# Kernel optimization log

Measured on AMD Instinct MI355X. Metric: run time of the kernel, lower is better.

The kernel has to match this reference:

```python
import jax, jax.numpy as jnp
import numpy as np

N = 50000      # nodes
F_IN = 128     # num_feat
HID = 128      # hidden size
OUT = 47       # num_out (classes)
E = 600000     # graph edges
EGO_E = 1200000  # concatenated egonet edges


def _linear_params(key, fan_in, fan_out):
    s = 1.0 / np.sqrt(fan_in)
    kw, kb = jax.random.split(key)
    W = jax.random.uniform(kw, (fan_in, fan_out), jnp.float32, -s, s)
    b = jax.random.uniform(kb, (fan_out,), jnp.float32, -s, s)
    return W, b


def setup_inputs() -> dict:
    key = jax.random.key(0)
    ks = jax.random.split(key, 8)
    x_in = jax.random.normal(ks[0], (N, F_IN), jnp.float32)
    edge_index_in = jax.random.randint(ks[1], (2, E), 0, N)
    ego_edge_index = jax.random.randint(ks[2], (2, EGO_E), 0, N)
    W_ego0, b_ego0 = _linear_params(ks[3], F_IN, F_IN)
    W_gin0, b_gin0 = _linear_params(ks[4], F_IN, HID)
    W_ego1, b_ego1 = _linear_params(ks[5], HID, HID)
    W_gin1, b_gin1 = _linear_params(ks[6], HID, OUT)
    return {
        "x_in": x_in, "edge_index_in": edge_index_in, "ego_edge_index": ego_edge_index,
        "W_ego0": W_ego0, "b_ego0": b_ego0, "W_gin0": W_gin0, "b_gin0": b_gin0,
        "W_ego1": W_ego1, "b_ego1": b_ego1, "W_gin1": W_gin1, "b_gin1": b_gin1,
    }


def reference(x_in, edge_index_in, ego_edge_index,
              W_ego0, b_ego0, W_gin0, b_gin0,
              W_ego1, b_ego1, W_gin1, b_gin1):
    n = x_in.shape[0]
    ego_row, ego_col = ego_edge_index[0], ego_edge_index[1]
    src, tgt = edge_index_in[0], edge_index_in[1]

    def do_conv(x):
        # sum_i spmm(A_i, x) == scatter-add over concatenated egonet edges, then / N
        return jax.ops.segment_sum(x[ego_col], ego_row, num_segments=n) * (1.0 / n)

    def gin(x, W, b):
        # GINConv(nn=Linear), eps=0: Linear(x + sum_{j->i} x_j)
        aggr = jax.ops.segment_sum(x[src], tgt, num_segments=n)
        return (x + aggr) @ W + b

    # layer 0: ['Ego','GIN', relu_mid=True, relu_end=True]
    x = do_conv(x_in) @ W_ego0 + b_ego0
    x = jax.nn.relu(x)
    x = gin(x, W_gin0, b_gin0)
    x = jax.nn.relu(x)
    # layer 1: ['Ego','GIN', relu_mid=True, relu_end=False]
    x = do_conv(x) @ W_ego1 + b_ego1
    x = jax.nn.relu(x)
    x = gin(x, W_gin1, b_gin1)
    return jax.nn.log_softmax(x, axis=1)
```

## Files before the change

kernel.cpp:

```cpp
#include <hip/hip_runtime.h>

#define SCAP_EGO 8192
#define SCAP_E   4096

typedef unsigned short ushort_t;
typedef unsigned int uint_t;
typedef __attribute__((ext_vector_type(8))) short bf16x8;
typedef __attribute__((ext_vector_type(4))) float f32x4;

__device__ inline float lo16(uint_t u) { return __uint_as_float(u << 16); }
__device__ inline float hi16(uint_t u) { return __uint_as_float(u & 0xFFFF0000u); }
__device__ inline ushort_t f2bf(float f) {
    uint_t i = __float_as_uint(f);
    return (ushort_t)((i + 0x7FFFu + ((i >> 16) & 1u)) >> 16);
}
__device__ inline uint_t pack2(float a, float b) {
    return (uint_t)f2bf(a) | ((uint_t)f2bf(b) << 16);
}
union U8 { uint4 u; bf16x8 v; };

__global__ __launch_bounds__(256) void prep(
    const float* __restrict__ x, ushort_t* __restrict__ xb, int n8,
    const float* __restrict__ W0, const float* __restrict__ W1,
    const float* __restrict__ W2, const float* __restrict__ W3,
    ushort_t* __restrict__ T0, ushort_t* __restrict__ T1,
    ushort_t* __restrict__ T2, ushort_t* __restrict__ T3,
    int* __restrict__ z)
{
    int i = blockIdx.x * 256 + threadIdx.x;
    if (i < 128) ((int4*)z)[i] = make_int4(0, 0, 0, 0);
    if (i < n8) {
        const float4* p = (const float4*)(x + (size_t)i * 8);
        float4 a = p[0], b = p[1];
        uint4 o;
        o.x = pack2(a.x, a.y); o.y = pack2(a.z, a.w);
        o.z = pack2(b.x, b.y); o.w = pack2(b.z, b.w);
        *(uint4*)(xb + (size_t)i * 8) = o;
    }
    if (i < 49152) {
        int mi = i >> 14;
        int r = i & 16383;
        int n = r >> 7, k = r & 127;
        const float* W = mi == 0 ? W0 : (mi == 1 ? W1 : W2);
        ushort_t* T = mi == 0 ? T0 : (mi == 1 ? T1 : T2);
        T[n * 128 + k] = f2bf(W[k * 128 + n]);
    } else if (i < 49152 + 6144) {
        int r = i - 49152;
        int n = r >> 7, k = r & 127;
        T3[n * 128 + k] = (n < 47) ? f2bf(W3[k * 47 + n]) : (ushort_t)0;
    }
}

__global__ __launch_bounds__(256) void bin_edges(
    const int* __restrict__ dst, const int* __restrict__ src, int nE, int scap,
    int* __restrict__ bincur, int2* __restrict__ stage)
{
    __shared__ int bcnt[256];
    __shared__ int gbase[256];
    int t = threadIdx.x;
    bcnt[t] = 0;
    __syncthreads();
    int base = blockIdx.x * 4096;
    int d[16], s[16], l[16];
#pragma unroll
    for (int i = 0; i < 16; i++) {
        int e = base + t + i * 256;
        if (e < nE) {
            d[i] = dst[e]; s[i] = src[e];
            l[i] = atomicAdd(&bcnt[d[i] >> 8], 1);
        } else d[i] = -1;
    }
    __syncthreads();
    if (bcnt[t]) gbase[t] = atomicAdd(&bincur[t], bcnt[t]);
    __syncthreads();
#pragma unroll
    for (int i = 0; i < 16; i++) {
        if (d[i] >= 0) {
            int b = d[i] >> 8;
            int slot = gbase[b] + l[i];
            if (slot < scap) stage[(size_t)b * scap + slot] = make_int2(d[i], s[i]);
        }
    }
}

__global__ __launch_bounds__(256) void build_csr(
    const int* __restrict__ bincur, const int2* __restrict__ stage, int scap,
    int* __restrict__ cnt, int* __restrict__ rowptr, int* __restrict__ packed,
    int nNodes)
{
    __shared__ int sc[256];
    __shared__ int wcur[256];
    int b = blockIdx.x, t = threadIdx.x;
    int m = bincur[b]; if (m > scap) m = scap;
    const int2* st = stage + (size_t)b * scap;
    sc[t] = 0;
    __syncthreads();
    for (int e = t; e < m; e += 256) atomicAdd(&sc[st[e].x & 255], 1);
    __syncthreads();
    int v = sc[t];
    __syncthreads();
    sc[t] = v;
    __syncthreads();
    for (int off = 1; off < 256; off <<= 1) {
        int y = (t >= off) ? sc[t - off] : 0;
        __syncthreads();
        sc[t] += y;
        __syncthreads();
    }
    int excl = sc[t] - v;
    int node = b * 256 + t;
    if (node < nNodes) { cnt[node] = v; rowptr[node] = b * scap + excl; }
    wcur[t] = excl;
    __syncthreads();
    int* pk = packed + (size_t)b * scap;
    for (int e = t; e < m; e += 256) {
        int2 p = st[e];
        int slot = atomicAdd(&wcur[p.x & 255], 1);
        pk[slot] = p.y;
    }
}

__global__ __launch_bounds__(256) void gather_bf(
    const ushort_t* __restrict__ x, const int* __restrict__ cnt,
    const int* __restrict__ rowptr, const int* __restrict__ packed,
    ushort_t* __restrict__ outb, int nNodes, float scale, int selfAdd)
{
    int g = threadIdx.x >> 5, lane = threadIdx.x & 31;
    int n = blockIdx.x * 8 + g;
    if (n >= nNodes) return;
    int len = cnt[n];
    const int* row = packed + rowptr[n];
    const ushort_t* base = x + lane * 4;
    float a0 = 0.f, a1 = 0.f, a2 = 0.f, a3 = 0.f;
    int e = 0;
    for (; e + 3 < len; e += 4) {
        int s0 = row[e], s1 = row[e + 1], s2 = row[e + 2], s3 = row[e + 3];
        uint2 w0 = *(const uint2*)(base + (size_t)s0 * 128);
        uint2 w1 = *(const uint2*)(base + (size_t)s1 * 128);
        uint2 w2 = *(const uint2*)(base + (size_t)s2 * 128);
        uint2 w3 = *(const uint2*)(base + (size_t)s3 * 128);
        a0 += lo16(w0.x) + lo16(w1.x) + lo16(w2.x) + lo16(w3.x);
        a1 += hi16(w0.x) + hi16(w1.x) + hi16(w2.x) + hi16(w3.x);
        a2 += lo16(w0.y) + lo16(w1.y) + lo16(w2.y) + lo16(w3.y);
        a3 += hi16(w0.y) + hi16(w1.y) + hi16(w2.y) + hi16(w3.y);
    }
    for (; e < len; e++) {
        uint2 w = *(const uint2*)(base + (size_t)row[e] * 128);
        a0 += lo16(w.x); a1 += hi16(w.x); a2 += lo16(w.y); a3 += hi16(w.y);
    }
    if (selfAdd) {
        uint2 w = *(const uint2*)(base + (size_t)n * 128);
        a0 += lo16(w.x); a1 += hi16(w.x); a2 += lo16(w.y); a3 += hi16(w.y);
    }
    uint2 o;
    o.x = pack2(a0 * scale, a1 * scale);
    o.y = pack2(a2 * scale, a3 * scale);
    *(uint2*)(outb + (size_t)n * 128 + lane * 4) = o;
}

template<bool RELU>
__global__ __launch_bounds__(256) void gemm_mfma(
    const ushort_t* __restrict__ A, const ushort_t* __restrict__ WT,
    const float* __restrict__ bias, ushort_t* __restrict__ outb, int nrows)
{
    __shared__ ushort_t Ws[128][136];
    int t = threadIdx.x;
    for (int j = t; j < 128 * 16; j += 256) {
        int n = j >> 4, kq = (j & 15) << 3;
        *(uint4*)&Ws[n][kq] = *(const uint4*)(WT + n * 128 + kq);
    }
    int wave = t >> 6, lane = t & 63;
    int m = lane & 15, quad = lane >> 4;
    int rowBase = blockIdx.x * 64 + wave * 16;
    int arow = rowBase + m; if (arow >= nrows) arow = 0;
    bf16x8 afr[4];
#pragma unroll
    for (int kt = 0; kt < 4; kt++) {
        U8 u; u.u = *(const uint4*)(A + (size_t)arow * 128 + kt * 32 + quad * 8);
        afr[kt] = u.v;
    }
    __syncthreads();
    f32x4 acc[8];
#pragma unroll
    for (int ct = 0; ct < 8; ct++) acc[ct] = (f32x4){0.f, 0.f, 0.f, 0.f};
#pragma unroll
    for (int ct = 0; ct < 8; ct++) {
#pragma unroll
        for (int kt = 0; kt < 4; kt++) {
            bf16x8 b = *(const bf16x8*)&Ws[ct * 16 + m][kt * 32 + quad * 8];
            acc[ct] = __builtin_amdgcn_mfma_f32_16x16x32_bf16(afr[kt], b, acc[ct], 0, 0, 0);
        }
    }
#pragma unroll
    for (int ct = 0; ct < 8; ct++) {
        int col = ct * 16 + m;
        float bb = bias[col];
#pragma unroll
        for (int r = 0; r < 4; r++) {
            int row = rowBase + quad * 4 + r;
            if (row < nrows) {
                float v = acc[ct][r] + bb;
                if (RELU) v = fmaxf(v, 0.f);
                outb[(size_t)row * 128 + col] = f2bf(v);
            }
        }
    }
}

__global__ __launch_bounds__(256) void gemm47_lsm(
    const ushort_t* __restrict__ A, const ushort_t* __restrict__ WT,
    const float* __restrict__ bias, float* __restrict__ out, int nrows)
{
    __shared__ ushort_t Ws[48][136];
    int t = threadIdx.x;
    for (int j = t; j < 48 * 16; j += 256) {
        int n = j >> 4, kq = (j & 15) << 3;
        *(uint4*)&Ws[n][kq] = *(const uint4*)(WT + n * 128 + kq);
    }
    int wave = t >> 6, lane = t & 63;
    int m = lane & 15, quad = lane >> 4;
    int rowBase = blockIdx.x * 64 + wave * 16;
    int arow = rowBase + m; if (arow >= nrows) arow = 0;
    bf16x8 afr[4];
#pragma unroll
    for (int kt = 0; kt < 4; kt++) {
        U8 u; u.u = *(const uint4*)(A + (size_t)arow * 128 + kt * 32 + quad * 8);
        afr[kt] = u.v;
    }
    __syncthreads();
    f32x4 acc[3];
#pragma unroll
    for (int ct = 0; ct < 3; ct++) acc[ct] = (f32x4){0.f, 0.f, 0.f, 0.f};
#pragma unroll
    for (int ct = 0; ct < 3; ct++) {
#pragma unroll
        for (int kt = 0; kt < 4; kt++) {
            bf16x8 b = *(const bf16x8*)&Ws[ct * 16 + m][kt * 32 + quad * 8];
            acc[ct] = __builtin_amdgcn_mfma_f32_16x16x32_bf16(afr[kt], b, acc[ct], 0, 0, 0);
        }
    }
    int c0 = m, c1 = 16 + m, c2 = 32 + m;
    bool has2 = (c2 < 47);
    float b0 = bias[c0], b1 = bias[c1], b2 = has2 ? bias[c2] : 0.f;
#pragma unroll
    for (int r = 0; r < 4; r++) {
        int row = rowBase + quad * 4 + r;
        float v0 = acc[0][r] + b0;
        float v1 = acc[1][r] + b1;
        float v2 = has2 ? (acc[2][r] + b2) : -INFINITY;
        float mx = fmaxf(fmaxf(v0, v1), v2);
#pragma unroll
        for (int off = 8; off; off >>= 1) mx = fmaxf(mx, __shfl_xor(mx, off, 64));
        float s = __expf(v0 - mx) + __expf(v1 - mx) + (has2 ? __expf(v2 - mx) : 0.f);
#pragma unroll
        for (int off = 8; off; off >>= 1) s += __shfl_xor(s, off, 64);
        float lse = mx + __logf(s);
        if (row < nrows) {
            float* o = out + (size_t)row * 47;
            o[c0] = v0 - lse;
            o[c1] = v1 - lse;
            if (has2) o[c2] = v2 - lse;
        }
    }
}

extern "C" void kernel_launch(void* const* d_in, const int* in_sizes, int n_in,
                              void* d_out, int out_size, void* d_ws, size_t ws_size,
                              hipStream_t stream) {
    const float* x_in   = (const float*)d_in[0];
    const int*   edge   = (const int*)d_in[1];
    const int*   ego    = (const int*)d_in[2];
    const float* W_ego0 = (const float*)d_in[3];
    const float* b_ego0 = (const float*)d_in[4];
    const float* W_gin0 = (const float*)d_in[5];
    const float* b_gin0 = (const float*)d_in[6];
    const float* W_ego1 = (const float*)d_in[7];
    const float* b_ego1 = (const float*)d_in[8];
    const float* W_gin1 = (const float*)d_in[9];
    const float* b_gin1 = (const float*)d_in[10];
    float* out = (float*)d_out;

    const int N     = in_sizes[0] / 128;
    const int E     = in_sizes[1] / 2;
    const int EGO_E = in_sizes[2] / 2;
    const float invN = 1.0f / (float)N;
    const int NB    = (N + 255) >> 8;

    const size_t NBELEM = (size_t)N * 128;
    ushort_t* Xb = (ushort_t*)d_ws;
    ushort_t* G  = Xb + NBELEM;
    ushort_t* H  = G + NBELEM;
    ushort_t* T0 = H + NBELEM;
    ushort_t* T1 = T0 + 16384;
    ushort_t* T2 = T1 + 16384;
    ushort_t* T3 = T2 + 16384;
    int* ip = (int*)(T3 + 6144);
    int* cnt_ego  = ip;              ip += N;
    int* rp_ego   = ip;              ip += N;
    int* cnt_edge = ip;              ip += N;
    int* rp_edge  = ip;              ip += N;
    int* bincur   = ip;              ip += 512;
    int2* stage_ego  = (int2*)ip;    ip += (size_t)NB * SCAP_EGO * 2;
    int*  pk_ego     = ip;           ip += (size_t)NB * SCAP_EGO;
    int2* stage_edge = (int2*)ip;    ip += (size_t)NB * SCAP_E * 2;
    int*  pk_edge    = ip;           ip += (size_t)NB * SCAP_E;

    const int gGemm  = (N + 63) / 64;
    const int gNode8 = (N + 7) / 8;
    const int gBinE  = (EGO_E + 4095) / 4096;
    const int gBinF  = (E + 4095) / 4096;
    const int gCvt   = ((N * 128 / 8) + 255) / 256;

    prep<<<gCvt, 256, 0, stream>>>(x_in, Xb, N * 128 / 8,
                                   W_ego0, W_gin0, W_ego1, W_gin1,
                                   T0, T1, T2, T3, bincur);
    bin_edges<<<gBinE, 256, 0, stream>>>(ego, ego + EGO_E, EGO_E, SCAP_EGO, bincur, stage_ego);
    bin_edges<<<gBinF, 256, 0, stream>>>(edge + E, edge, E, SCAP_E, bincur + 256, stage_edge);
    build_csr<<<NB, 256, 0, stream>>>(bincur, stage_ego, SCAP_EGO, cnt_ego, rp_ego, pk_ego, N);
    build_csr<<<NB, 256, 0, stream>>>(bincur + 256, stage_edge, SCAP_E, cnt_edge, rp_edge, pk_edge, N);

    gather_bf<<<gNode8, 256, 0, stream>>>(Xb, cnt_ego, rp_ego, pk_ego, G, N, invN, 0);
    gemm_mfma<true><<<gGemm, 256, 0, stream>>>(G, T0, b_ego0, H, N);
    gather_bf<<<gNode8, 256, 0, stream>>>(H, cnt_edge, rp_edge, pk_edge, G, N, 1.f, 1);
    gemm_mfma<true><<<gGemm, 256, 0, stream>>>(G, T1, b_gin0, H, N);
    gather_bf<<<gNode8, 256, 0, stream>>>(H, cnt_ego, rp_ego, pk_ego, G, N, invN, 0);
    gemm_mfma<true><<<gGemm, 256, 0, stream>>>(G, T2, b_ego1, H, N);
    gather_bf<<<gNode8, 256, 0, stream>>>(H, cnt_edge, rp_edge, pk_edge, G, N, 1.f, 1);
    gemm47_lsm<<<gGemm, 256, 0, stream>>>(G, T3, b_gin1, out, N);
}
```

Before: 338.0 us.

## Fuse sparse gather into MFMA GEMM kernels via shared-memory staging

Each gather-then-GEMM pair becomes one kernel. A 64-row block gathers and aggregates neighbour rows into an LDS tile, then runs the MFMA GEMM on it, so the intermediate bf16 matrix is never written to or read back from global memory and four launches are removed. The gather now uses 16 lanes per row with 16-byte loads instead of 32 lanes with 8-byte loads. In exchange the 256-thread block walks 64 rows, 4 per 16-lane group, serially, which lowers the parallelism available to the latency-bound gather. LDS use per block also rises, which may reduce occupancy.

```diff
diff --git a/kernel.cpp b/kernel.cpp
--- a/kernel.cpp
+++ b/kernel.cpp
@@ -120,66 +120,86 @@
     }
 }
 
-__global__ __launch_bounds__(256) void gather_bf(
-    const ushort_t* __restrict__ x, const int* __restrict__ cnt,
-    const int* __restrict__ rowptr, const int* __restrict__ packed,
-    ushort_t* __restrict__ outb, int nNodes, float scale, int selfAdd)
-{
-    int g = threadIdx.x >> 5, lane = threadIdx.x & 31;
-    int n = blockIdx.x * 8 + g;
-    if (n >= nNodes) return;
-    int len = cnt[n];
-    const int* row = packed + rowptr[n];
-    const ushort_t* base = x + lane * 4;
-    float a0 = 0.f, a1 = 0.f, a2 = 0.f, a3 = 0.f;
+__device__ inline void gather_row(
+    const ushort_t* __restrict__ base, const int* __restrict__ row, int len,
+    float* a)
+{
+#pragma unroll
+    for (int m = 0; m < 8; m++) a[m] = 0.f;
     int e = 0;
     for (; e + 3 < len; e += 4) {
         int s0 = row[e], s1 = row[e + 1], s2 = row[e + 2], s3 = row[e + 3];
-        uint2 w0 = *(const uint2*)(base + (size_t)s0 * 128);
-        uint2 w1 = *(const uint2*)(base + (size_t)s1 * 128);
-        uint2 w2 = *(const uint2*)(base + (size_t)s2 * 128);
-        uint2 w3 = *(const uint2*)(base + (size_t)s3 * 128);
-        a0 += lo16(w0.x) + lo16(w1.x) + lo16(w2.x) + lo16(w3.x);
-        a1 += hi16(w0.x) + hi16(w1.x) + hi16(w2.x) + hi16(w3.x);
-        a2 += lo16(w0.y) + lo16(w1.y) + lo16(w2.y) + lo16(w3.y);
-        a3 += hi16(w0.y) + hi16(w1.y) + hi16(w2.y) + hi16(w3.y);
+        uint4 w0 = *(const uint4*)(base + (size_t)s0 * 128);
+        uint4 w1 = *(const uint4*)(base + (size_t)s1 * 128);
+        uint4 w2 = *(const uint4*)(base + (size_t)s2 * 128);
+        uint4 w3 = *(const uint4*)(base + (size_t)s3 * 128);
+        a[0] += lo16(w0.x) + lo16(w1.x) + lo16(w2.x) + lo16(w3.x);
+        a[1] += hi16(w0.x) + hi16(w1.x) + hi16(w2.x) + hi16(w3.x);
+        a[2] += lo16(w0.y) + lo16(w1.y) + lo16(w2.y) + lo16(w3.y);
+        a[3] += hi16(w0.y) + hi16(w1.y) + hi16(w2.y) + hi16(w3.y);
+        a[4] += lo16(w0.z) + lo16(w1.z) + lo16(w2.z) + lo16(w3.z);
+        a[5] += hi16(w0.z) + hi16(w1.z) + hi16(w2.z) + hi16(w3.z);
+        a[6] += lo16(w0.w) + lo16(w1.w) + lo16(w2.w) + lo16(w3.w);
+        a[7] += hi16(w0.w) + hi16(w1.w) + hi16(w2.w) + hi16(w3.w);
     }
     for (; e < len; e++) {
-        uint2 w = *(const uint2*)(base + (size_t)row[e] * 128);
-        a0 += lo16(w.x); a1 += hi16(w.x); a2 += lo16(w.y); a3 += hi16(w.y);
-    }
-    if (selfAdd) {
-        uint2 w = *(const uint2*)(base + (size_t)n * 128);
-        a0 += lo16(w.x); a1 += hi16(w.x); a2 += lo16(w.y); a3 += hi16(w.y);
-    }
-    uint2 o;
-    o.x = pack2(a0 * scale, a1 * scale);
-    o.y = pack2(a2 * scale, a3 * scale);
-    *(uint2*)(outb + (size_t)n * 128 + lane * 4) = o;
-}
-
-template<bool RELU>
-__global__ __launch_bounds__(256) void gemm_mfma(
-    const ushort_t* __restrict__ A, const ushort_t* __restrict__ WT,
-    const float* __restrict__ bias, ushort_t* __restrict__ outb, int nrows)
+        uint4 w = *(const uint4*)(base + (size_t)row[e] * 128);
+        a[0] += lo16(w.x); a[1] += hi16(w.x);
+        a[2] += lo16(w.y); a[3] += hi16(w.y);
+        a[4] += lo16(w.z); a[5] += hi16(w.z);
+        a[6] += lo16(w.w); a[7] += hi16(w.w);
+    }
+}
+
+template<bool RELU, bool SELF>
+__global__ __launch_bounds__(256) void gg128(
+    const ushort_t* __restrict__ x, const int* __restrict__ cnt,
+    const int* __restrict__ rowptr, const int* __restrict__ packed,
+    const ushort_t* __restrict__ WT, const float* __restrict__ bias,
+    ushort_t* __restrict__ outb, int nrows, float scale)
 {
     __shared__ ushort_t Ws[128][136];
+    __shared__ ushort_t Ag[64][136];
     int t = threadIdx.x;
     for (int j = t; j < 128 * 16; j += 256) {
         int n = j >> 4, kq = (j & 15) << 3;
         *(uint4*)&Ws[n][kq] = *(const uint4*)(WT + n * 128 + kq);
     }
-    int wave = t >> 6, lane = t & 63;
-    int m = lane & 15, quad = lane >> 4;
+    int g = t >> 4, lane = t & 15;
+    const ushort_t* base = x + lane * 8;
+#pragma unroll
+    for (int rr = 0; rr < 4; rr++) {
+        int lrow = g * 4 + rr;
+        int n = blockIdx.x * 64 + lrow;
+        float a[8];
+        if (n < nrows) {
+            gather_row(base, packed + rowptr[n], cnt[n], a);
+            if (SELF) {
+                uint4 w = *(const uint4*)(base + (size_t)n * 128);
+                a[0] += lo16(w.x); a[1] += hi16(w.x);
+                a[2] += lo16(w.y); a[3] += hi16(w.y);
+                a[4] += lo16(w.z); a[5] += hi16(w.z);
+                a[6] += lo16(w.w); a[7] += hi16(w.w);
+            }
+        } else {
+#pragma unroll
+            for (int m = 0; m < 8; m++) a[m] = 0.f;
+        }
+        uint4 o;
+        o.x = pack2(a[0] * scale, a[1] * scale);
+        o.y = pack2(a[2] * scale, a[3] * scale);
+        o.z = pack2(a[4] * scale, a[5] * scale);
+        o.w = pack2(a[6] * scale, a[7] * scale);
+        *(uint4*)&Ag[lrow][lane * 8] = o;
+    }
+    __syncthreads();
+    int wave = t >> 6, l64 = t & 63;
+    int m = l64 & 15, quad = l64 >> 4;
     int rowBase = blockIdx.x * 64 + wave * 16;
-    int arow = rowBase + m; if (arow >= nrows) arow = 0;
     bf16x8 afr[4];
 #pragma unroll
-    for (int kt = 0; kt < 4; kt++) {
-        U8 u; u.u = *(const uint4*)(A + (size_t)arow * 128 + kt * 32 + quad * 8);
-        afr[kt] = u.v;
-    }
-    __syncthreads();
+    for (int kt = 0; kt < 4; kt++)
+        afr[kt] = *(const bf16x8*)&Ag[wave * 16 + m][kt * 32 + quad * 8];
     f32x4 acc[8];
 #pragma unroll
     for (int ct = 0; ct < 8; ct++) acc[ct] = (f32x4){0.f, 0.f, 0.f, 0.f};
@@ -207,27 +227,50 @@
     }
 }
 
-__global__ __launch_bounds__(256) void gemm47_lsm(
-    const ushort_t* __restrict__ A, const ushort_t* __restrict__ WT,
-    const float* __restrict__ bias, float* __restrict__ out, int nrows)
+__global__ __launch_bounds__(256) void gg47_lsm(
+    const ushort_t* __restrict__ x, const int* __restrict__ cnt,
+    const int* __restrict__ rowptr, const int* __restrict__ packed,
+    const ushort_t* __restrict__ WT, const float* __restrict__ bias,
+    float* __restrict__ out, int nrows)
 {
     __shared__ ushort_t Ws[48][136];
+    __shared__ ushort_t Ag[64][136];
     int t = threadIdx.x;
     for (int j = t; j < 48 * 16; j += 256) {
         int n = j >> 4, kq = (j & 15) << 3;
         *(uint4*)&Ws[n][kq] = *(const uint4*)(WT + n * 128 + kq);
     }
-    int wave = t >> 6, lane = t & 63;
-    int m = lane & 15, quad = lane >> 4;
+    int g = t >> 4, lane = t & 15;
+    const ushort_t* base = x + lane * 8;
+#pragma unroll
+    for (int rr = 0; rr < 4; rr++) {
+        int lrow = g * 4 + rr;
+        int n = blockIdx.x * 64 + lrow;
+        float a[8];
+        if (n < nrows) {
+            gather_row(base, packed + rowptr[n], cnt[n], a);
+            uint4 w = *(const uint4*)(base + (size_t)n * 128);
+            a[0] += lo16(w.x); a[1] += hi16(w.x);
+            a[2] += lo16(w.y); a[3] += hi16(w.y);
+            a[4] += lo16(w.z); a[5] += hi16(w.z);
+            a[6] += lo16(w.w); a[7] += hi16(w.w);
+        } else {
+#pragma unroll
+            for (int m = 0; m < 8; m++) a[m] = 0.f;
+        }
+        uint4 o;
+        o.x = pack2(a[0], a[1]); o.y = pack2(a[2], a[3]);
+        o.z = pack2(a[4], a[5]); o.w = pack2(a[6], a[7]);
+        *(uint4*)&Ag[lrow][lane * 8] = o;
+    }
+    __syncthreads();
+    int wave = t >> 6, l64 = t & 63;
+    int m = l64 & 15, quad = l64 >> 4;
     int rowBase = blockIdx.x * 64 + wave * 16;
-    int arow = rowBase + m; if (arow >= nrows) arow = 0;
     bf16x8 afr[4];
 #pragma unroll
-    for (int kt = 0; kt < 4; kt++) {
-        U8 u; u.u = *(const uint4*)(A + (size_t)arow * 128 + kt * 32 + quad * 8);
-        afr[kt] = u.v;
-    }
-    __syncthreads();
+    for (int kt = 0; kt < 4; kt++)
+        afr[kt] = *(const bf16x8*)&Ag[wave * 16 + m][kt * 32 + quad * 8];
     f32x4 acc[3];
 #pragma unroll
     for (int ct = 0; ct < 3; ct++) acc[ct] = (f32x4){0.f, 0.f, 0.f, 0.f};
@@ -288,9 +331,9 @@
 
     const size_t NBELEM = (size_t)N * 128;
     ushort_t* Xb = (ushort_t*)d_ws;
-    ushort_t* G  = Xb + NBELEM;
-    ushort_t* H  = G + NBELEM;
-    ushort_t* T0 = H + NBELEM;
+    ushort_t* A1 = Xb + NBELEM;
+    ushort_t* A2 = A1 + NBELEM;
+    ushort_t* T0 = A2 + NBELEM;
     ushort_t* T1 = T0 + 16384;
     ushort_t* T2 = T1 + 16384;
     ushort_t* T3 = T2 + 16384;
@@ -305,11 +348,10 @@
     int2* stage_edge = (int2*)ip;    ip += (size_t)NB * SCAP_E * 2;
     int*  pk_edge    = ip;           ip += (size_t)NB * SCAP_E;
 
-    const int gGemm  = (N + 63) / 64;
-    const int gNode8 = (N + 7) / 8;
-    const int gBinE  = (EGO_E + 4095) / 4096;
-    const int gBinF  = (E + 4095) / 4096;
-    const int gCvt   = ((N * 128 / 8) + 255) / 256;
+    const int gGG   = (N + 63) / 64;
+    const int gBinE = (EGO_E + 4095) / 4096;
+    const int gBinF = (E + 4095) / 4096;
+    const int gCvt  = ((N * 128 / 8) + 255) / 256;
 
     prep<<<gCvt, 256, 0, stream>>>(x_in, Xb, N * 128 / 8,
                                    W_ego0, W_gin0, W_ego1, W_gin1,
@@ -319,12 +361,12 @@
     build_csr<<<NB, 256, 0, stream>>>(bincur, stage_ego, SCAP_EGO, cnt_ego, rp_ego, pk_ego, N);
     build_csr<<<NB, 256, 0, stream>>>(bincur + 256, stage_edge, SCAP_E, cnt_edge, rp_edge, pk_edge, N);
 
-    gather_bf<<<gNode8, 256, 0, stream>>>(Xb, cnt_ego, rp_ego, pk_ego, G, N, invN, 0);
-    gemm_mfma<true><<<gGemm, 256, 0, stream>>>(G, T0, b_ego0, H, N);
-    gather_bf<<<gNode8, 256, 0, stream>>>(H, cnt_edge, rp_edge, pk_edge, G, N, 1.f, 1);
-    gemm_mfma<true><<<gGemm, 256, 0, stream>>>(G, T1, b_gin0, H, N);
-    gather_bf<<<gNode8, 256, 0, stream>>>(H, cnt_ego, rp_ego, pk_ego, G, N, invN, 0);
-    gemm_mfma<true><<<gGemm, 256, 0, stream>>>(G, T2, b_ego1, H, N);
-    gather_bf<<<gNode8, 256, 0, stream>>>(H, cnt_edge, rp_edge, pk_edge, G, N, 1.f, 1);
-    gemm47_lsm<<<gGemm, 256, 0, stream>>>(G, T3, b_gin1, out, N);
-}
+    gg128<true, false><<<gGG, 256, 0, stream>>>(Xb, cnt_ego, rp_ego, pk_ego,
+                                                T0, b_ego0, A1, N, invN);
+    gg128<true, true><<<gGG, 256, 0, stream>>>(A1, cnt_edge, rp_edge, pk_edge,
+                                               T1, b_gin0, A2, N, 1.f);
+    gg128<true, false><<<gGG, 256, 0, stream>>>(A2, cnt_ego, rp_ego, pk_ego,
+                                                T2, b_ego1, A1, N, invN);
+    gg47_lsm<<<gGG, 256, 0, stream>>>(A1, cnt_edge, rp_edge, pk_edge,
+                                      T3, b_gin1, out, N);
+}
```

New measurement: 398.2 us. +17.8%, slower.
